# Kernel optimization log

Hardware: AMD Instinct MI355X
Metric: run time of the kernel (lower is better)

## Reference

```python
import jax, jax.numpy as jnp
import numpy as np

LOG2 = float(np.log(2.0))

def ssp(v):
    # shifted softplus: log(0.5*e^v + 0.5)
    return jax.nn.softplus(v) - jnp.asarray(LOG2, v.dtype)

def lora_dense(h, W, b, A, B):
    # base GEMM + per-sample (modulated) low-rank correction; scale = alpha/rank = 1
    base = jnp.einsum('b...i,io->b...o', h, W) + b
    lora = jnp.einsum('b...r,bro->b...o', jnp.einsum('b...i,bir->b...r', h, A), B)
    return ssp(base + lora)

def setup_inputs() -> dict:
    key = jax.random.key(0)
    ks = jax.random.split(key, 32)
    Bsz, Atoms, F, Rbf, R = 2, 512, 128, 64, 4
    d = {}
    d['x'] = jax.random.normal(ks[0], (Bsz, Atoms, F), jnp.float32)
    d['f_ij'] = jax.random.uniform(ks[1], (Bsz, Atoms, Atoms, Rbf), jnp.float32)
    d['c_ij'] = jax.random.uniform(ks[2], (Bsz, Atoms, Atoms), jnp.float32)
    d['mask'] = jax.random.randint(ks[3], (Bsz, Atoms, Atoms), 0, 2, jnp.int32)
    def mk(i, din, dout):
        return (jax.random.normal(ks[4+4*i], (din, dout), jnp.float32) * (1.0/np.sqrt(din)),
                jnp.zeros((dout,), jnp.float32),
                jax.random.normal(ks[5+4*i], (Bsz, din, R), jnp.float32) * 0.05,
                jax.random.normal(ks[6+4*i], (Bsz, R, dout), jnp.float32) * 0.05)
    d['W_bc'], d['b_bc'], d['A_bc'], d['B_bc'] = mk(0, F, F)      # atomwise_bc: F -> dim_filter(=F)
    d['W_f0'], d['b_f0'], d['A_f0'], d['B_f0'] = mk(1, Rbf, F)    # dis_filter layer0
    d['W_f1'], d['b_f1'], d['A_f1'], d['B_f1'] = mk(2, F, F)      # dis_filter layer1
    d['W_f2'], d['b_f2'], d['A_f2'], d['B_f2'] = mk(3, F, F)      # dis_filter layer2
    d['W_a0'], d['b_a0'], d['A_a0'], d['B_a0'] = mk(4, F, F)      # atomwise_ac layer0
    d['W_a1'], d['b_a1'], d['A_a1'], d['B_a1'] = mk(5, F, F)      # atomwise_ac layer1
    return d

def reference(x, f_ij, c_ij, mask,
              W_bc, b_bc, A_bc, B_bc,
              W_f0, b_f0, A_f0, B_f0,
              W_f1, b_f1, A_f1, B_f1,
              W_f2, b_f2, A_f2, B_f2,
              W_a0, b_a0, A_a0, B_a0,
              W_a1, b_a1, A_a1, B_a1):
    x_i = lora_dense(x, W_bc, b_bc, A_bc, B_bc)                 # (B, A, Fdim)
    h = lora_dense(f_ij, W_f0, b_f0, A_f0, B_f0)                # (B, A, A, Fdim)
    h = lora_dense(h, W_f1, b_f1, A_f1, B_f1)
    h = lora_dense(h, W_f2, b_f2, A_f2, B_f2)
    w_ij = h * c_ij[..., None]                                  # (B, A, A, Fdim)
    # x_ij = expand_dims(x_i, -3): neighbor-j features broadcast over receiver i
    y = x_i[:, None, :, :] * w_ij                               # (B, A, A, Fdim)
    y = y * mask[..., None].astype(y.dtype)
    y = jnp.sum(y, axis=-2)                                     # masked neighbor sum -> (B, A, Fdim)
    y = lora_dense(y, W_a0, b_a0, A_a0, B_a0)
    y = lora_dense(y, W_a1, b_a1, A_a1, B_a1)
    return x + y
```

## Files before the change

### kernel.cpp

```cpp
#include <hip/hip_runtime.h>
#include <hip/hip_bf16.h>


typedef float        f32x4  __attribute__((ext_vector_type(4)));
typedef unsigned int u32x4  __attribute__((ext_vector_type(4)));
typedef unsigned int u32x2  __attribute__((ext_vector_type(2)));
typedef __bf16       bf16x8 __attribute__((ext_vector_type(8)));

__device__ __forceinline__ float ssp_f(float v) {
  return __logf(0.5f * __expf(v) + 0.5f);
}

__device__ __forceinline__ unsigned short f2bfu(float f) {
  __hip_bfloat16 h = __float2bfloat16(f);
  return __builtin_bit_cast(unsigned short, h);
}

__device__ __forceinline__ u32x4 pack8(f32x4 a, f32x4 b) {
  u32x4 u;
  u.x = (unsigned)f2bfu(a.x) | ((unsigned)f2bfu(a.y) << 16);
  u.y = (unsigned)f2bfu(a.z) | ((unsigned)f2bfu(a.w) << 16);
  u.z = (unsigned)f2bfu(b.x) | ((unsigned)f2bfu(b.y) << 16);
  u.w = (unsigned)f2bfu(b.z) | ((unsigned)f2bfu(b.w) << 16);
  return u;
}

__device__ __forceinline__ f32x4 fzero4() { f32x4 z = {0.f, 0.f, 0.f, 0.f}; return z; }

#define SWZ(j) (((j) & 7) << 4)

__global__ void prep_weights(
    const float* __restrict__ W_bc, const float* __restrict__ A_bc, const float* __restrict__ B_bc,
    const float* __restrict__ W_f0, const float* __restrict__ A_f0, const float* __restrict__ B_f0,
    const float* __restrict__ W_f1, const float* __restrict__ A_f1, const float* __restrict__ B_f1,
    const float* __restrict__ W_f2, const float* __restrict__ A_f2, const float* __restrict__ B_f2,
    const float* __restrict__ W_a0, const float* __restrict__ A_a0, const float* __restrict__ B_a0,
    const float* __restrict__ W_a1, const float* __restrict__ A_a1, const float* __restrict__ B_a1,
    unsigned short* __restrict__ Wt0, unsigned short* __restrict__ Wt1, unsigned short* __restrict__ Wt2,
    float* __restrict__ Wbc, float* __restrict__ Wa0, float* __restrict__ Wa1)
{
  const int l = blockIdx.y, b = blockIdx.z;
  const int e = blockIdx.x * 256 + threadIdx.x;
  const float *W, *A, *Bm; int din;
  switch (l) {
    case 0:  W = W_bc; A = A_bc; Bm = B_bc; din = 128; break;
    case 1:  W = W_f0; A = A_f0; Bm = B_f0; din = 64;  break;
    case 2:  W = W_f1; A = A_f1; Bm = B_f1; din = 128; break;
    case 3:  W = W_f2; A = A_f2; Bm = B_f2; din = 128; break;
    case 4:  W = W_a0; A = A_a0; Bm = B_a0; din = 128; break;
    default: W = W_a1; A = A_a1; Bm = B_a1; din = 128; break;
  }
  if (e >= din * 128) return;
  const int k = e >> 7, n = e & 127;
  float wv = W[k * 128 + n];
  #pragma unroll
  for (int r = 0; r < 4; ++r)
    wv += A[(b * din + k) * 4 + r] * Bm[(b * 4 + r) * 128 + n];
  if (l == 1)      Wt0[(b * 128 + n) * 64  + k] = f2bfu(wv);
  else if (l == 2) Wt1[(b * 128 + n) * 128 + k] = f2bfu(wv);
  else if (l == 3) Wt2[(b * 128 + n) * 128 + k] = f2bfu(wv);
  else if (l == 0) Wbc[(b * 128 + k) * 128 + n] = wv;
  else if (l == 4) Wa0[(b * 128 + k) * 128 + n] = wv;
  else             Wa1[(b * 128 + k) * 128 + n] = wv;
}

__global__ __launch_bounds__(512) void dense_ssp(
    const float* __restrict__ in, const float* __restrict__ W,
    const float* __restrict__ bias, const float* __restrict__ resid,
    float* __restrict__ out)
{
  __shared__ float in_l[4][128];
  const int t = threadIdx.x;
  const int rg0 = blockIdx.x << 2;
  const int b = rg0 >> 9;
  in_l[t >> 7][t & 127] = in[rg0 * 128 + t];
  __syncthreads();
  const int j = t >> 7, n = t & 127;
  const float* wp = W + (b << 14) + n;
  const float* ip = in_l[j];
  float acc = 0.f;
  #pragma unroll 8
  for (int k = 0; k < 128; ++k) acc += ip[k] * wp[k << 7];
  float r = ssp_f(acc + bias[n]);
  const int oi = (rg0 + j) * 128 + n;
  if (resid) r += resid[oi];
  out[oi] = r;
}

__global__ __launch_bounds__(256, 2) void schnet_core(
    const float* __restrict__ f_ij, const float* __restrict__ c_ij,
    const int* __restrict__ mask,
    const unsigned short* __restrict__ Wt0, const unsigned short* __restrict__ Wt1,
    const unsigned short* __restrict__ Wt2,
    const float* __restrict__ bias0, const float* __restrict__ bias1,
    const float* __restrict__ bias2,
    const float* __restrict__ xi, float* __restrict__ y)
{
  __shared__ __align__(16) unsigned short fbuf[64 * 64];
  __shared__ __align__(16) unsigned short hbuf[64 * 128];
  __shared__ int   jlist[576];
  __shared__ float slist[576];
  __shared__ int cnt_s[8], base_s[8], nact_s;

  const int tid  = threadIdx.x;
  const int lane = tid & 63;
  const int w    = tid >> 6;
  const int lrow = lane & 15;
  const int lgrp = lane >> 4;
  const int bi   = blockIdx.x;
  const int b    = bi >> 9;

  const int mb = bi << 9;
  const int jA = tid, jB = tid + 256;
  const int   mA = mask[mb + jA]; const float cA = c_ij[mb + jA];
  const int   mB = mask[mb + jB]; const float cB = c_ij[mb + jB];
  unsigned long long balA = __ballot(mA != 0);
  unsigned long long balB = __ballot(mB != 0);
  if (lane == 0) { cnt_s[w] = __popcll(balA); cnt_s[4 + w] = __popcll(balB); }
  __syncthreads();
  if (tid == 0) {
    int s = 0;
    for (int c = 0; c < 8; ++c) { base_s[c] = s; s += cnt_s[c]; }
    nact_s = s;
  }
  __syncthreads();
  const int na = nact_s;
  const unsigned long long lm = (1ull << lane) - 1ull;
  if (mA) { int p = base_s[w]     + __popcll(balA & lm); jlist[p] = jA; slist[p] = cA; }
  if (mB) { int p = base_s[4 + w] + __popcll(balB & lm); jlist[p] = jB; slist[p] = cB; }
  if (tid < 64) { int idx = na + tid; if (idx < 576) { jlist[idx] = 0; slist[idx] = 0.f; } }
  __syncthreads();

  const int mg = w;
  bf16x8 w0f[2][2], w1f[2][4], w2f[2][4];
  f32x4  bs0[2], bs1[2], bs2[2];
  #pragma unroll
  for (int nt = 0; nt < 2; ++nt) {
    const int nout = mg * 32 + nt * 16 + lrow;
    const int nb0 = (b * 128 + nout) * 64  + lgrp * 8;
    const int nb1 = (b * 128 + nout) * 128 + lgrp * 8;
    #pragma unroll
    for (int ks = 0; ks < 2; ++ks)
      w0f[nt][ks] = *(const bf16x8*)(Wt0 + nb0 + ks * 32);
    #pragma unroll
    for (int ks = 0; ks < 4; ++ks) {
      w1f[nt][ks] = *(const bf16x8*)(Wt1 + nb1 + ks * 32);
      w2f[nt][ks] = *(const bf16x8*)(Wt2 + nb1 + ks * 32);
    }
    const int n0 = mg * 32 + nt * 16 + lgrp * 4;
    bs0[nt] = *(const f32x4*)(bias0 + n0);
    bs1[nt] = *(const f32x4*)(bias1 + n0);
    bs2[nt] = *(const f32x4*)(bias2 + n0);
  }

  float accy[2][4] = {{0.f,0.f,0.f,0.f},{0.f,0.f,0.f,0.f}};
  const float* fbase = f_ij + ((size_t)mb << 6);

  for (int jt0 = 0; jt0 < na; jt0 += 64) {
    {
      const int r = tid >> 2, part = tid & 3;
      const int ja = jlist[jt0 + r];
      const f32x4* src = (const f32x4*)(fbase + ja * 64 + part * 16);
      f32x4 v0 = src[0], v1 = src[1], v2 = src[2], v3 = src[3];
      char* dst = (char*)fbuf + r * 128;
      const int o0 = (part * 32) ^ SWZ(r);
      *(u32x4*)(dst + o0)        = pack8(v0, v1);
      *(u32x4*)(dst + (o0 ^ 16)) = pack8(v2, v3);
    }
    __syncthreads();

    f32x4 acc[2][4];

    #pragma unroll
    for (int nt = 0; nt < 2; ++nt)
      #pragma unroll
      for (int jt = 0; jt < 4; ++jt) acc[nt][jt] = fzero4();
    #pragma unroll
    for (int jt = 0; jt < 4; ++jt) {
      const int j = jt * 16 + lrow;
      const char* rb = (const char*)fbuf + j * 128;
      const int sw = SWZ(j);
      #pragma unroll
      for (int ks = 0; ks < 2; ++ks) {
        bf16x8 bf = *(const bf16x8*)(rb + ((lgrp * 16 + ks * 64) ^ sw));
        acc[0][jt] = __builtin_amdgcn_mfma_f32_16x16x32_bf16(w0f[0][ks], bf, acc[0][jt], 0, 0, 0);
        acc[1][jt] = __builtin_amdgcn_mfma_f32_16x16x32_bf16(w0f[1][ks], bf, acc[1][jt], 0, 0, 0);
      }
    }
    #pragma unroll
    for (int jt = 0; jt < 4; ++jt) {
      const int j = jt * 16 + lrow;
      char* rb = (char*)hbuf + j * 256;
      const int sw = SWZ(j);
      #pragma unroll
      for (int nt = 0; nt < 2; ++nt) {
        const int n0 = mg * 32 + nt * 16 + lgrp * 4;
        float e0 = ssp_f(acc[nt][jt].x + bs0[nt].x);
        float e1 = ssp_f(acc[nt][jt].y + bs0[nt].y);
        float e2 = ssp_f(acc[nt][jt].z + bs0[nt].z);
        float e3 = ssp_f(acc[nt][jt].w + bs0[nt].w);
        u32x2 pk;
        pk.x = (unsigned)f2bfu(e0) | ((unsigned)f2bfu(e1) << 16);
        pk.y = (unsigned)f2bfu(e2) | ((unsigned)f2bfu(e3) << 16);
        *(u32x2*)(rb + ((n0 * 2) ^ sw)) = pk;
      }
    }
    __syncthreads();

    #pragma unroll
    for (int nt = 0; nt < 2; ++nt)
      #pragma unroll
      for (int jt = 0; jt < 4; ++jt) acc[nt][jt] = fzero4();
    #pragma unroll
    for (int jt = 0; jt < 4; ++jt) {
      const int j = jt * 16 + lrow;
      const char* rb = (const char*)hbuf + j * 256;
      const int sw = SWZ(j);
      #pragma unroll
      for (int ks = 0; ks < 4; ++ks) {
        bf16x8 bf = *(const bf16x8*)(rb + ((lgrp * 16 + ks * 64) ^ sw));
        acc[0][jt] = __builtin_amdgcn_mfma_f32_16x16x32_bf16(w1f[0][ks], bf, acc[0][jt], 0, 0, 0);
        acc[1][jt] = __builtin_amdgcn_mfma_f32_16x16x32_bf16(w1f[1][ks], bf, acc[1][jt], 0, 0, 0);
      }
    }
    __syncthreads();
    #pragma unroll
    for (int jt = 0; jt < 4; ++jt) {
      const int j = jt * 16 + lrow;
      char* rb = (char*)hbuf + j * 256;
      const int sw = SWZ(j);
      #pragma unroll
      for (int nt = 0; nt < 2; ++nt) {
        const int n0 = mg * 32 + nt * 16 + lgrp * 4;
        float e0 = ssp_f(acc[nt][jt].x + bs1[nt].x);
        float e1 = ssp_f(acc[nt][jt].y + bs1[nt].y);
        float e2 = ssp_f(acc[nt][jt].z + bs1[nt].z);
        float e3 = ssp_f(acc[nt][jt].w + bs1[nt].w);
        u32x2 pk;
        pk.x = (unsigned)f2bfu(e0) | ((unsigned)f2bfu(e1) << 16);
        pk.y = (unsigned)f2bfu(e2) | ((unsigned)f2bfu(e3) << 16);
        *(u32x2*)(rb + ((n0 * 2) ^ sw)) = pk;
      }
    }
    __syncthreads();

    #pragma unroll
    for (int nt = 0; nt < 2; ++nt)
      #pragma unroll
      for (int jt = 0; jt < 4; ++jt) acc[nt][jt] = fzero4();
    #pragma unroll
    for (int jt = 0; jt < 4; ++jt) {
      const int j = jt * 16 + lrow;
      const char* rb = (const char*)hbuf + j * 256;
      const int sw = SWZ(j);
      #pragma unroll
      for (int ks = 0; ks < 4; ++ks) {
        bf16x8 bf = *(const bf16x8*)(rb + ((lgrp * 16 + ks * 64) ^ sw));
        acc[0][jt] = __builtin_amdgcn_mfma_f32_16x16x32_bf16(w2f[0][ks], bf, acc[0][jt], 0, 0, 0);
        acc[1][jt] = __builtin_amdgcn_mfma_f32_16x16x32_bf16(w2f[1][ks], bf, acc[1][jt], 0, 0, 0);
      }
    }
    #pragma unroll
    for (int jt = 0; jt < 4; ++jt) {
      const int jj = jt * 16 + lrow;
      const float s  = slist[jt0 + jj];
      const int   ja = jlist[jt0 + jj];
      const float* xr = xi + (((b << 9) + ja) << 7);
      #pragma unroll
      for (int nt = 0; nt < 2; ++nt) {
        const int n0 = mg * 32 + nt * 16 + lgrp * 4;
        f32x4 xv = *(const f32x4*)(xr + n0);
        float h0 = ssp_f(acc[nt][jt].x + bs2[nt].x);
        float h1 = ssp_f(acc[nt][jt].y + bs2[nt].y);
        float h2 = ssp_f(acc[nt][jt].z + bs2[nt].z);
        float h3 = ssp_f(acc[nt][jt].w + bs2[nt].w);
        accy[nt][0] += s * xv.x * h0;
        accy[nt][1] += s * xv.y * h1;
        accy[nt][2] += s * xv.z * h2;
        accy[nt][3] += s * xv.w * h3;
      }
    }
  }

  #pragma unroll
  for (int d = 1; d < 16; d <<= 1)
    #pragma unroll
    for (int nt = 0; nt < 2; ++nt)
      #pragma unroll
      for (int r = 0; r < 4; ++r)
        accy[nt][r] += __shfl_xor(accy[nt][r], d, 64);
  if (lrow == 0) {
    float* yo = y + ((size_t)bi << 7);
    #pragma unroll
    for (int nt = 0; nt < 2; ++nt) {
      const int n0 = mg * 32 + nt * 16 + lgrp * 4;
      f32x4 v = {accy[nt][0], accy[nt][1], accy[nt][2], accy[nt][3]};
      *(f32x4*)(yo + n0) = v;
    }
  }
}

extern "C" void kernel_launch(void* const* d_in, const int* in_sizes, int n_in,
                              void* d_out, int out_size, void* d_ws, size_t ws_size,
                              hipStream_t stream)
{
  const float* x    = (const float*)d_in[0];
  const float* f_ij = (const float*)d_in[1];
  const float* c_ij = (const float*)d_in[2];
  const int*   mask = (const int*)d_in[3];
  const float* W_bc = (const float*)d_in[4];
  const float* b_bc = (const float*)d_in[5];
  const float* A_bc = (const float*)d_in[6];
  const float* B_bc = (const float*)d_in[7];
  const float* W_f0 = (const float*)d_in[8];
  const float* b_f0 = (const float*)d_in[9];
  const float* A_f0 = (const float*)d_in[10];
  const float* B_f0 = (const float*)d_in[11];
  const float* W_f1 = (const float*)d_in[12];
  const float* b_f1 = (const float*)d_in[13];
  const float* A_f1 = (const float*)d_in[14];
  const float* B_f1 = (const float*)d_in[15];
  const float* W_f2 = (const float*)d_in[16];
  const float* b_f2 = (const float*)d_in[17];
  const float* A_f2 = (const float*)d_in[18];
  const float* B_f2 = (const float*)d_in[19];
  const float* W_a0 = (const float*)d_in[20];
  const float* b_a0 = (const float*)d_in[21];
  const float* A_a0 = (const float*)d_in[22];
  const float* B_a0 = (const float*)d_in[23];
  const float* W_a1 = (const float*)d_in[24];
  const float* b_a1 = (const float*)d_in[25];
  const float* A_a1 = (const float*)d_in[26];
  const float* B_a1 = (const float*)d_in[27];
  float* out = (float*)d_out;

  char* ws = (char*)d_ws;
  unsigned short* Wt0 = (unsigned short*)(ws);
  unsigned short* Wt1 = (unsigned short*)(ws + 32768);
  unsigned short* Wt2 = (unsigned short*)(ws + 98304);
  float* Wbc = (float*)(ws + 163840);
  float* Wa0 = (float*)(ws + 294912);
  float* Wa1 = (float*)(ws + 425984);
  float* xi  = (float*)(ws + 557056);
  float* yb  = (float*)(ws + 1081344);
  float* y1  = (float*)(ws + 1605632);

  prep_weights<<<dim3(64, 6, 2), 256, 0, stream>>>(
      W_bc, A_bc, B_bc, W_f0, A_f0, B_f0, W_f1, A_f1, B_f1,
      W_f2, A_f2, B_f2, W_a0, A_a0, B_a0, W_a1, A_a1, B_a1,
      Wt0, Wt1, Wt2, Wbc, Wa0, Wa1);

  dense_ssp<<<256, 512, 0, stream>>>(x, Wbc, b_bc, nullptr, xi);

  schnet_core<<<1024, 256, 0, stream>>>(f_ij, c_ij, mask, Wt0, Wt1, Wt2,
                                        b_f0, b_f1, b_f2, xi, yb);

  dense_ssp<<<256, 512, 0, stream>>>(yb, Wa0, b_a0, nullptr, y1);
  dense_ssp<<<256, 512, 0, stream>>>(y1, Wa1, b_a1, x, out);
}
```

Baseline: 118.3 us.

## Split neighbor tiles across two blocks per row and reload weights per stage

Each receiver row's active-neighbor tiles are now split between two blocks, doubling the grid, and each block writes a partial sum that the next dense layer adds on load. Per-lane weight fragments are no longer held in registers for the whole loop; they are reloaded from global or L2 before each MFMA stage, which lowers register pressure so launch bounds can request 4 blocks per SIMD. The softplus uses raw exp2 and log intrinsics with the bias pre-scaled by log2(e) and kept in LDS. The costs are repeated weight loads per tile, duplicated mask compaction in both halves, an extra sync per tile, and extra partial-sum traffic.

```diff
diff --git a/kernel.cpp b/kernel.cpp
--- a/kernel.cpp
+++ b/kernel.cpp
@@ -7,8 +7,14 @@
 typedef unsigned int u32x2  __attribute__((ext_vector_type(2)));
 typedef __bf16       bf16x8 __attribute__((ext_vector_type(8)));
 
+__device__ __forceinline__ float ssp_pre(float acc, float bpre) {
+  float t = __builtin_amdgcn_exp2f(__builtin_fmaf(acc, 1.44269504089f, bpre));
+  return 0.69314718056f * __builtin_amdgcn_logf(__builtin_fmaf(t, 0.5f, 0.5f));
+}
+
 __device__ __forceinline__ float ssp_f(float v) {
-  return __logf(0.5f * __expf(v) + 0.5f);
+  float t = __builtin_amdgcn_exp2f(v * 1.44269504089f);
+  return 0.69314718056f * __builtin_amdgcn_logf(__builtin_fmaf(t, 0.5f, 0.5f));
 }
 
 __device__ __forceinline__ unsigned short f2bfu(float f) {
@@ -65,15 +71,19 @@
 }
 
 __global__ __launch_bounds__(512) void dense_ssp(
-    const float* __restrict__ in, const float* __restrict__ W,
-    const float* __restrict__ bias, const float* __restrict__ resid,
-    float* __restrict__ out)
+    const float* __restrict__ in, const float* __restrict__ in2,
+    const float* __restrict__ W, const float* __restrict__ bias,
+    const float* __restrict__ resid, float* __restrict__ out)
 {
   __shared__ float in_l[4][128];
   const int t = threadIdx.x;
   const int rg0 = blockIdx.x << 2;
   const int b = rg0 >> 9;
-  in_l[t >> 7][t & 127] = in[rg0 * 128 + t];
+  {
+    float v = in[rg0 * 128 + t];
+    if (in2) v += in2[rg0 * 128 + t];
+    in_l[t >> 7][t & 127] = v;
+  }
   __syncthreads();
   const int j = t >> 7, n = t & 127;
   const float* wp = W + (b << 14) + n;
@@ -87,19 +97,20 @@
   out[oi] = r;
 }
 
-__global__ __launch_bounds__(256, 2) void schnet_core(
+__global__ __launch_bounds__(256, 4) void schnet_core(
     const float* __restrict__ f_ij, const float* __restrict__ c_ij,
     const int* __restrict__ mask,
     const unsigned short* __restrict__ Wt0, const unsigned short* __restrict__ Wt1,
     const unsigned short* __restrict__ Wt2,
     const float* __restrict__ bias0, const float* __restrict__ bias1,
     const float* __restrict__ bias2,
-    const float* __restrict__ xi, float* __restrict__ y)
+    const float* __restrict__ xi, float* __restrict__ ypart)
 {
   __shared__ __align__(16) unsigned short fbuf[64 * 64];
   __shared__ __align__(16) unsigned short hbuf[64 * 128];
   __shared__ int   jlist[576];
   __shared__ float slist[576];
+  __shared__ float bias_l[384];
   __shared__ int cnt_s[8], base_s[8], nact_s;
 
   const int tid  = threadIdx.x;
@@ -107,8 +118,15 @@
   const int w    = tid >> 6;
   const int lrow = lane & 15;
   const int lgrp = lane >> 4;
-  const int bi   = blockIdx.x;
+  const int g    = blockIdx.x;
+  const int bi   = g >> 1;
+  const int h    = g & 1;
   const int b    = bi >> 9;
+
+  for (int t = tid; t < 384; t += 256) {
+    const float* bp = (t < 128) ? bias0 : (t < 256) ? bias1 : bias2;
+    bias_l[t] = bp[t & 127] * 1.44269504089f;
+  }
 
   const int mb = bi << 9;
   const int jA = tid, jB = tid + 256;
@@ -131,32 +149,20 @@
   if (tid < 64) { int idx = na + tid; if (idx < 576) { jlist[idx] = 0; slist[idx] = 0.f; } }
   __syncthreads();
 
+  const int tiles = (na + 63) >> 6;
+  const int tmid  = (tiles + 1) >> 1;
+  const int t0 = h ? tmid : 0;
+  const int t1 = h ? tiles : tmid;
+
   const int mg = w;
-  bf16x8 w0f[2][2], w1f[2][4], w2f[2][4];
-  f32x4  bs0[2], bs1[2], bs2[2];
-  #pragma unroll
-  for (int nt = 0; nt < 2; ++nt) {
-    const int nout = mg * 32 + nt * 16 + lrow;
-    const int nb0 = (b * 128 + nout) * 64  + lgrp * 8;
-    const int nb1 = (b * 128 + nout) * 128 + lgrp * 8;
-    #pragma unroll
-    for (int ks = 0; ks < 2; ++ks)
-      w0f[nt][ks] = *(const bf16x8*)(Wt0 + nb0 + ks * 32);
-    #pragma unroll
-    for (int ks = 0; ks < 4; ++ks) {
-      w1f[nt][ks] = *(const bf16x8*)(Wt1 + nb1 + ks * 32);
-      w2f[nt][ks] = *(const bf16x8*)(Wt2 + nb1 + ks * 32);
-    }
-    const int n0 = mg * 32 + nt * 16 + lgrp * 4;
-    bs0[nt] = *(const f32x4*)(bias0 + n0);
-    bs1[nt] = *(const f32x4*)(bias1 + n0);
-    bs2[nt] = *(const f32x4*)(bias2 + n0);
-  }
-
   float accy[2][4] = {{0.f,0.f,0.f,0.f},{0.f,0.f,0.f,0.f}};
   const float* fbase = f_ij + ((size_t)mb << 6);
 
-  for (int jt0 = 0; jt0 < na; jt0 += 64) {
+  const int wbase0 = ((b << 7) + mg * 32 + lrow) * 64  + (lgrp << 3);
+  const int wbase1 = ((b << 7) + mg * 32 + lrow) * 128 + (lgrp << 3);
+
+  for (int tt = t0; tt < t1; ++tt) {
+    const int jt0 = tt << 6;
     {
       const int r = tid >> 2, part = tid & 3;
       const int ja = jlist[jt0 + r];
@@ -171,115 +177,161 @@
 
     f32x4 acc[2][4];
 
-    #pragma unroll
-    for (int nt = 0; nt < 2; ++nt)
-      #pragma unroll
-      for (int jt = 0; jt < 4; ++jt) acc[nt][jt] = fzero4();
-    #pragma unroll
-    for (int jt = 0; jt < 4; ++jt) {
-      const int j = jt * 16 + lrow;
-      const char* rb = (const char*)fbuf + j * 128;
-      const int sw = SWZ(j);
-      #pragma unroll
-      for (int ks = 0; ks < 2; ++ks) {
-        bf16x8 bf = *(const bf16x8*)(rb + ((lgrp * 16 + ks * 64) ^ sw));
-        acc[0][jt] = __builtin_amdgcn_mfma_f32_16x16x32_bf16(w0f[0][ks], bf, acc[0][jt], 0, 0, 0);
-        acc[1][jt] = __builtin_amdgcn_mfma_f32_16x16x32_bf16(w0f[1][ks], bf, acc[1][jt], 0, 0, 0);
-      }
-    }
-    #pragma unroll
-    for (int jt = 0; jt < 4; ++jt) {
-      const int j = jt * 16 + lrow;
-      char* rb = (char*)hbuf + j * 256;
-      const int sw = SWZ(j);
-      #pragma unroll
-      for (int nt = 0; nt < 2; ++nt) {
-        const int n0 = mg * 32 + nt * 16 + lgrp * 4;
-        float e0 = ssp_f(acc[nt][jt].x + bs0[nt].x);
-        float e1 = ssp_f(acc[nt][jt].y + bs0[nt].y);
-        float e2 = ssp_f(acc[nt][jt].z + bs0[nt].z);
-        float e3 = ssp_f(acc[nt][jt].w + bs0[nt].w);
-        u32x2 pk;
-        pk.x = (unsigned)f2bfu(e0) | ((unsigned)f2bfu(e1) << 16);
-        pk.y = (unsigned)f2bfu(e2) | ((unsigned)f2bfu(e3) << 16);
-        *(u32x2*)(rb + ((n0 * 2) ^ sw)) = pk;
+    {
+      const unsigned short* wp = Wt0 + wbase0;
+      asm volatile("" : "+v"(wp));
+      bf16x8 wf[2][2];
+      #pragma unroll
+      for (int nt = 0; nt < 2; ++nt)
+        #pragma unroll
+        for (int ks = 0; ks < 2; ++ks)
+          wf[nt][ks] = *(const bf16x8*)(wp + nt * (16 * 64) + ks * 32);
+      #pragma unroll
+      for (int nt = 0; nt < 2; ++nt)
+        #pragma unroll
+        for (int jt = 0; jt < 4; ++jt) acc[nt][jt] = fzero4();
+      #pragma unroll
+      for (int jt = 0; jt < 4; ++jt) {
+        const int j = jt * 16 + lrow;
+        const char* rb = (const char*)fbuf + j * 128;
+        const int sw = SWZ(j);
+        #pragma unroll
+        for (int ks = 0; ks < 2; ++ks) {
+          bf16x8 bf = *(const bf16x8*)(rb + ((lgrp * 16 + ks * 64) ^ sw));
+          acc[0][jt] = __builtin_amdgcn_mfma_f32_16x16x32_bf16(wf[0][ks], bf, acc[0][jt], 0, 0, 0);
+          acc[1][jt] = __builtin_amdgcn_mfma_f32_16x16x32_bf16(wf[1][ks], bf, acc[1][jt], 0, 0, 0);
+        }
+      }
+    }
+    {
+      f32x4 bp0 = *(const f32x4*)(bias_l +       mg * 32 + 0  + lgrp * 4);
+      f32x4 bp1 = *(const f32x4*)(bias_l +       mg * 32 + 16 + lgrp * 4);
+      #pragma unroll
+      for (int jt = 0; jt < 4; ++jt) {
+        const int j = jt * 16 + lrow;
+        char* rb = (char*)hbuf + j * 256;
+        const int sw = SWZ(j);
+        #pragma unroll
+        for (int nt = 0; nt < 2; ++nt) {
+          const int n0 = mg * 32 + nt * 16 + lgrp * 4;
+          const f32x4 bp = nt ? bp1 : bp0;
+          float e0 = ssp_pre(acc[nt][jt].x, bp.x);
+          float e1 = ssp_pre(acc[nt][jt].y, bp.y);
+          float e2 = ssp_pre(acc[nt][jt].z, bp.z);
+          float e3 = ssp_pre(acc[nt][jt].w, bp.w);
+          u32x2 pk;
+          pk.x = (unsigned)f2bfu(e0) | ((unsigned)f2bfu(e1) << 16);
+          pk.y = (unsigned)f2bfu(e2) | ((unsigned)f2bfu(e3) << 16);
+          *(u32x2*)(rb + ((n0 * 2) ^ sw)) = pk;
+        }
       }
     }
     __syncthreads();
 
-    #pragma unroll
-    for (int nt = 0; nt < 2; ++nt)
-      #pragma unroll
-      for (int jt = 0; jt < 4; ++jt) acc[nt][jt] = fzero4();
-    #pragma unroll
-    for (int jt = 0; jt < 4; ++jt) {
-      const int j = jt * 16 + lrow;
-      const char* rb = (const char*)hbuf + j * 256;
-      const int sw = SWZ(j);
-      #pragma unroll
-      for (int ks = 0; ks < 4; ++ks) {
-        bf16x8 bf = *(const bf16x8*)(rb + ((lgrp * 16 + ks * 64) ^ sw));
-        acc[0][jt] = __builtin_amdgcn_mfma_f32_16x16x32_bf16(w1f[0][ks], bf, acc[0][jt], 0, 0, 0);
-        acc[1][jt] = __builtin_amdgcn_mfma_f32_16x16x32_bf16(w1f[1][ks], bf, acc[1][jt], 0, 0, 0);
+    {
+      const unsigned short* wp = Wt1 + wbase1;
+      asm volatile("" : "+v"(wp));
+      bf16x8 wf[2][4];
+      #pragma unroll
+      for (int nt = 0; nt < 2; ++nt)
+        #pragma unroll
+        for (int ks = 0; ks < 4; ++ks)
+          wf[nt][ks] = *(const bf16x8*)(wp + nt * (16 * 128) + ks * 32);
+      #pragma unroll
+      for (int nt = 0; nt < 2; ++nt)
+        #pragma unroll
+        for (int jt = 0; jt < 4; ++jt) acc[nt][jt] = fzero4();
+      #pragma unroll
+      for (int jt = 0; jt < 4; ++jt) {
+        const int j = jt * 16 + lrow;
+        const char* rb = (const char*)hbuf + j * 256;
+        const int sw = SWZ(j);
+        #pragma unroll
+        for (int ks = 0; ks < 4; ++ks) {
+          bf16x8 bf = *(const bf16x8*)(rb + ((lgrp * 16 + ks * 64) ^ sw));
+          acc[0][jt] = __builtin_amdgcn_mfma_f32_16x16x32_bf16(wf[0][ks], bf, acc[0][jt], 0, 0, 0);
+          acc[1][jt] = __builtin_amdgcn_mfma_f32_16x16x32_bf16(wf[1][ks], bf, acc[1][jt], 0, 0, 0);
+        }
       }
     }
     __syncthreads();
-    #pragma unroll
-    for (int jt = 0; jt < 4; ++jt) {
-      const int j = jt * 16 + lrow;
-      char* rb = (char*)hbuf + j * 256;
-      const int sw = SWZ(j);
-      #pragma unroll
-      for (int nt = 0; nt < 2; ++nt) {
-        const int n0 = mg * 32 + nt * 16 + lgrp * 4;
-        float e0 = ssp_f(acc[nt][jt].x + bs1[nt].x);
-        float e1 = ssp_f(acc[nt][jt].y + bs1[nt].y);
-        float e2 = ssp_f(acc[nt][jt].z + bs1[nt].z);
-        float e3 = ssp_f(acc[nt][jt].w + bs1[nt].w);
-        u32x2 pk;
-        pk.x = (unsigned)f2bfu(e0) | ((unsigned)f2bfu(e1) << 16);
-        pk.y = (unsigned)f2bfu(e2) | ((unsigned)f2bfu(e3) << 16);
-        *(u32x2*)(rb + ((n0 * 2) ^ sw)) = pk;
+    {
+      f32x4 bp0 = *(const f32x4*)(bias_l + 128 + mg * 32 + 0  + lgrp * 4);
+      f32x4 bp1 = *(const f32x4*)(bias_l + 128 + mg * 32 + 16 + lgrp * 4);
+      #pragma unroll
+      for (int jt = 0; jt < 4; ++jt) {
+        const int j = jt * 16 + lrow;
+        char* rb = (char*)hbuf + j * 256;
+        const int sw = SWZ(j);
+        #pragma unroll
+        for (int nt = 0; nt < 2; ++nt) {
+          const int n0 = mg * 32 + nt * 16 + lgrp * 4;
+          const f32x4 bp = nt ? bp1 : bp0;
+          float e0 = ssp_pre(acc[nt][jt].x, bp.x);
+          float e1 = ssp_pre(acc[nt][jt].y, bp.y);
+          float e2 = ssp_pre(acc[nt][jt].z, bp.z);
+          float e3 = ssp_pre(acc[nt][jt].w, bp.w);
+          u32x2 pk;
+          pk.x = (unsigned)f2bfu(e0) | ((unsigned)f2bfu(e1) << 16);
+          pk.y = (unsigned)f2bfu(e2) | ((unsigned)f2bfu(e3) << 16);
+          *(u32x2*)(rb + ((n0 * 2) ^ sw)) = pk;
+        }
       }
     }
     __syncthreads();
 
-    #pragma unroll
-    for (int nt = 0; nt < 2; ++nt)
-      #pragma unroll
-      for (int jt = 0; jt < 4; ++jt) acc[nt][jt] = fzero4();
-    #pragma unroll
-    for (int jt = 0; jt < 4; ++jt) {
-      const int j = jt * 16 + lrow;
-      const char* rb = (const char*)hbuf + j * 256;
-      const int sw = SWZ(j);
-      #pragma unroll
-      for (int ks = 0; ks < 4; ++ks) {
-        bf16x8 bf = *(const bf16x8*)(rb + ((lgrp * 16 + ks * 64) ^ sw));
-        acc[0][jt] = __builtin_amdgcn_mfma_f32_16x16x32_bf16(w2f[0][ks], bf, acc[0][jt], 0, 0, 0);
-        acc[1][jt] = __builtin_amdgcn_mfma_f32_16x16x32_bf16(w2f[1][ks], bf, acc[1][jt], 0, 0, 0);
-      }
-    }
-    #pragma unroll
-    for (int jt = 0; jt < 4; ++jt) {
-      const int jj = jt * 16 + lrow;
-      const float s  = slist[jt0 + jj];
-      const int   ja = jlist[jt0 + jj];
-      const float* xr = xi + (((b << 9) + ja) << 7);
-      #pragma unroll
-      for (int nt = 0; nt < 2; ++nt) {
-        const int n0 = mg * 32 + nt * 16 + lgrp * 4;
-        f32x4 xv = *(const f32x4*)(xr + n0);
-        float h0 = ssp_f(acc[nt][jt].x + bs2[nt].x);
-        float h1 = ssp_f(acc[nt][jt].y + bs2[nt].y);
-        float h2 = ssp_f(acc[nt][jt].z + bs2[nt].z);
-        float h3 = ssp_f(acc[nt][jt].w + bs2[nt].w);
-        accy[nt][0] += s * xv.x * h0;
-        accy[nt][1] += s * xv.y * h1;
-        accy[nt][2] += s * xv.z * h2;
-        accy[nt][3] += s * xv.w * h3;
-      }
-    }
+    {
+      const unsigned short* wp = Wt2 + wbase1;
+      asm volatile("" : "+v"(wp));
+      bf16x8 wf[2][4];
+      #pragma unroll
+      for (int nt = 0; nt < 2; ++nt)
+        #pragma unroll
+        for (int ks = 0; ks < 4; ++ks)
+          wf[nt][ks] = *(const bf16x8*)(wp + nt * (16 * 128) + ks * 32);
+      #pragma unroll
+      for (int nt = 0; nt < 2; ++nt)
+        #pragma unroll
+        for (int jt = 0; jt < 4; ++jt) acc[nt][jt] = fzero4();
+      #pragma unroll
+      for (int jt = 0; jt < 4; ++jt) {
+        const int j = jt * 16 + lrow;
+        const char* rb = (const char*)hbuf + j * 256;
+        const int sw = SWZ(j);
+        #pragma unroll
+        for (int ks = 0; ks < 4; ++ks) {
+          bf16x8 bf = *(const bf16x8*)(rb + ((lgrp * 16 + ks * 64) ^ sw));
+          acc[0][jt] = __builtin_amdgcn_mfma_f32_16x16x32_bf16(wf[0][ks], bf, acc[0][jt], 0, 0, 0);
+          acc[1][jt] = __builtin_amdgcn_mfma_f32_16x16x32_bf16(wf[1][ks], bf, acc[1][jt], 0, 0, 0);
+        }
+      }
+    }
+    {
+      f32x4 bp0 = *(const f32x4*)(bias_l + 256 + mg * 32 + 0  + lgrp * 4);
+      f32x4 bp1 = *(const f32x4*)(bias_l + 256 + mg * 32 + 16 + lgrp * 4);
+      #pragma unroll
+      for (int jt = 0; jt < 4; ++jt) {
+        const int jj = jt * 16 + lrow;
+        const float s  = slist[jt0 + jj];
+        const int   ja = jlist[jt0 + jj];
+        const float* xr = xi + (((b << 9) + ja) << 7);
+        #pragma unroll
+        for (int nt = 0; nt < 2; ++nt) {
+          const int n0 = mg * 32 + nt * 16 + lgrp * 4;
+          const f32x4 bp = nt ? bp1 : bp0;
+          f32x4 xv = *(const f32x4*)(xr + n0);
+          float h0 = ssp_pre(acc[nt][jt].x, bp.x);
+          float h1 = ssp_pre(acc[nt][jt].y, bp.y);
+          float h2 = ssp_pre(acc[nt][jt].z, bp.z);
+          float h3 = ssp_pre(acc[nt][jt].w, bp.w);
+          accy[nt][0] += s * xv.x * h0;
+          accy[nt][1] += s * xv.y * h1;
+          accy[nt][2] += s * xv.z * h2;
+          accy[nt][3] += s * xv.w * h3;
+        }
+      }
+    }
+    __syncthreads();
   }
 
   #pragma unroll
@@ -290,7 +342,7 @@
       for (int r = 0; r < 4; ++r)
         accy[nt][r] += __shfl_xor(accy[nt][r], d, 64);
   if (lrow == 0) {
-    float* yo = y + ((size_t)bi << 7);
+    float* yo = ypart + ((size_t)h << 17) + ((size_t)bi << 7);
     #pragma unroll
     for (int nt = 0; nt < 2; ++nt) {
       const int n0 = mg * 32 + nt * 16 + lgrp * 4;
@@ -342,19 +394,19 @@
   float* Wa0 = (float*)(ws + 294912);
   float* Wa1 = (float*)(ws + 425984);
   float* xi  = (float*)(ws + 557056);
-  float* yb  = (float*)(ws + 1081344);
-  float* y1  = (float*)(ws + 1605632);
+  float* yp  = (float*)(ws + 1081344);
+  float* y1  = (float*)(ws + 2129920);
 
   prep_weights<<<dim3(64, 6, 2), 256, 0, stream>>>(
       W_bc, A_bc, B_bc, W_f0, A_f0, B_f0, W_f1, A_f1, B_f1,
       W_f2, A_f2, B_f2, W_a0, A_a0, B_a0, W_a1, A_a1, B_a1,
       Wt0, Wt1, Wt2, Wbc, Wa0, Wa1);
 
-  dense_ssp<<<256, 512, 0, stream>>>(x, Wbc, b_bc, nullptr, xi);
-
-  schnet_core<<<1024, 256, 0, stream>>>(f_ij, c_ij, mask, Wt0, Wt1, Wt2,
-                                        b_f0, b_f1, b_f2, xi, yb);
-
-  dense_ssp<<<256, 512, 0, stream>>>(yb, Wa0, b_a0, nullptr, y1);
-  dense_ssp<<<256, 512, 0, stream>>>(y1, Wa1, b_a1, x, out);
-}
+  dense_ssp<<<256, 512, 0, stream>>>(x, nullptr, Wbc, b_bc, nullptr, xi);
+
+  schnet_core<<<2048, 256, 0, stream>>>(f_ij, c_ij, mask, Wt0, Wt1, Wt2,
+                                        b_f0, b_f1, b_f2, xi, yp);
+
+  dense_ssp<<<256, 512, 0, stream>>>(yp, yp + (1 << 17), Wa0, b_a0, nullptr, y1);
+  dense_ssp<<<256, 512, 0, stream>>>(y1, nullptr, Wa1, b_a1, x, out);
+}
```

Measured after the change: 113.3 us. 4.2% less time.
